# Performance work log

Hardware: AMD Instinct MI355X
Metric: run time of the kernel (lower is better)

The kernel has to match this reference:

```python
import jax, jax.numpy as jnp
import numpy as np

THRESHOLD = 20.0
CIRCLE_OFFSETS = [(0, -3), (1, -3), (2, -2), (3, -1), (3, 0), (3, 1), (2, 2), (1, 3),
                  (0, 3), (-1, 3), (-2, 2), (-3, 1), (-3, 0), (-3, -1), (-2, -2), (-1, -3)]


def setup_inputs() -> dict:
    key = jax.random.key(0)
    image = jax.random.uniform(key, (4, 1, 1080, 1920), dtype=jnp.float32) * 255.0
    return {"image": image}


def _detect_9_consecutive(bits_16):
    # bits_16: int32 (N, H, W). Build 24-bit circular buffer, test all 16 rotations
    # for 9 consecutive set bits (window == 511) using arithmetic-only ops.
    lower_8 = bits_16 % 256
    buffer_24 = bits_16 + lower_8 * 65536  # (N, H, W) int32
    divisors = (jnp.int32(2) ** jnp.arange(16, dtype=jnp.int32)).reshape(16, 1, 1, 1)
    shifted = (buffer_24[None] // divisors) % 512  # (16, N, H, W)
    return jnp.any(shifted == 511, axis=0)  # (N, H, W) bool


def reference(image):
    N, C, H, W = image.shape
    img = image.astype(jnp.float32)
    # Replicate-pad by 3 and gather the 16 Bresenham circle pixels via shifted slices.
    padded = jnp.pad(img[:, 0], ((0, 0), (3, 3), (3, 3)), mode='edge')  # (N, H+6, W+6)
    circle = jnp.stack(
        [padded[:, 3 + dy:3 + dy + H, 3 + dx:3 + dx + W] for dy, dx in CIRCLE_OFFSETS],
        axis=-1)  # (N, H, W, 16)
    center = img[:, 0][..., None]  # (N, H, W, 1)
    diff = circle - center
    powers = (jnp.int32(1) << jnp.arange(16, dtype=jnp.int32)).reshape(1, 1, 1, 16)
    dark_bits = ((diff >= THRESHOLD).astype(jnp.int32) * powers).sum(axis=-1)
    bright_bits = ((diff <= -THRESHOLD).astype(jnp.int32) * powers).sum(axis=-1)
    detected = _detect_9_consecutive(dark_bits) | _detect_9_consecutive(bright_bits)
    return detected.astype(jnp.float32)[:, None]  # (N, 1, H, W)
```

## Files before the change

### kernel.cpp

```cpp
#include <hip/hip_runtime.h>

#define IMG_H 1080
#define IMG_W 1920
#define TILE_W 128
#define TILE_H 32
#define SW 134
#define SH 38
#define SP 136

__device__ __forceinline__ unsigned det9(unsigned m) {
    unsigned x = m | (m << 16);
    unsigned t = x & (x >> 1);
    t &= t >> 2;
    t &= t >> 4;
    t &= x >> 8;
    return t & 0xFFFFu;
}

__global__ __launch_bounds__(256) void fast_score_kernel(const float* __restrict__ img,
                                                         float* __restrict__ out) {
    __shared__ float sm[SH * SP];

    const int n  = blockIdx.z;
    const int x0 = blockIdx.x * TILE_W;
    const int y0 = blockIdx.y * TILE_H;
    const int tid = threadIdx.x;

    const float* in = img + (size_t)n * (IMG_H * IMG_W);
    float* op = out + (size_t)n * (IMG_H * IMG_W);

    {
        const int lane = tid & 63;
        const int rgrp = tid >> 6;
        for (int r = rgrp; r < SH; r += 4) {
            int gy = y0 - 3 + r;
            gy = min(max(gy, 0), IMG_H - 1);
            const float* rowp = in + (size_t)gy * IMG_W;
            for (int c = lane; c < SW; c += 64) {
                int gx = x0 - 3 + c;
                gx = min(max(gx, 0), IMG_W - 1);
                sm[r * SP + c] = rowp[gx];
            }
        }
    }
    __syncthreads();

    const int cg = tid & 31;
    const int rg = tid >> 5;
    const int C = cg * 4;
    const int R = rg * 4;

    float wv[10][12];
#pragma unroll
    for (int r = 0; r < 10; ++r) {
        const float* sp = &sm[(R + r) * SP + C];
        float4 a = *(const float4*)(sp);
        float4 b = *(const float4*)(sp + 4);
        float4 c4 = *(const float4*)(sp + 8);
        wv[r][0] = a.x;  wv[r][1] = a.y;  wv[r][2]  = a.z;  wv[r][3]  = a.w;
        wv[r][4] = b.x;  wv[r][5] = b.y;  wv[r][6]  = b.z;  wv[r][7]  = b.w;
        wv[r][8] = c4.x; wv[r][9] = c4.y; wv[r][10] = c4.z; wv[r][11] = c4.w;
    }

    constexpr int DY[16] = {0, 1, 2, 3, 3, 3, 2, 1, 0, -1, -2, -3, -3, -3, -2, -1};
    constexpr int DX[16] = {-3, -3, -2, -1, 0, 1, 2, 3, 3, 3, 2, 1, 0, -1, -2, -3};

#pragma unroll
    for (int rr = 0; rr < 4; ++rr) {
        const int gy = y0 + R + rr;
        float4 res;
        float* resp = &res.x;
#pragma unroll
        for (int cc = 0; cc < 4; ++cc) {
            const float center = wv[rr + 3][cc + 3];
            unsigned dark = 0u, bright = 0u;
#pragma unroll
            for (int k = 0; k < 16; ++k) {
                const float d = wv[rr + 3 + DY[k]][cc + 3 + DX[k]] - center;
                dark   |= (d >=  20.0f ? 1u : 0u) << k;
                bright |= (d <= -20.0f ? 1u : 0u) << k;
            }
            resp[cc] = (det9(dark) | det9(bright)) ? 1.0f : 0.0f;
        }
        if (gy < IMG_H) {
            *(float4*)(op + (size_t)gy * IMG_W + (x0 + C)) = res;
        }
    }
}

extern "C" void kernel_launch(void* const* d_in, const int* in_sizes, int n_in,
                              void* d_out, int out_size, void* d_ws, size_t ws_size,
                              hipStream_t stream) {
    const float* img = (const float*)d_in[0];
    float* out = (float*)d_out;
    const int n_img = in_sizes[0] / (IMG_H * IMG_W);
    dim3 grid((IMG_W + TILE_W - 1) / TILE_W,
              (IMG_H + TILE_H - 1) / TILE_H,
              n_img);
    fast_score_kernel<<<grid, 256, 0, stream>>>(img, out);
}
```

Baseline: 114.6 us.

## Use rolling 7-row register window and precomputed thresholds in FAST kernel

Replaces the 10x12 register window with a 7-row ring buffer of float4s that is refilled from shared memory as each output row finishes, reducing live registers, and requests 4 blocks per CU through launch bounds. The threshold comparisons now test neighbours against precomputed center±20 instead of subtracting per neighbour. Bits are built by shift-in, which reverses bit order; the circular 9-run test is symmetric so the result is unchanged, and the 0xFFFF mask is dropped since only non-zero is tested. Comparing against center±20 instead of the difference may flip results on rare float rounding edge cases.

```diff
diff --git a/kernel.cpp b/kernel.cpp
--- a/kernel.cpp
+++ b/kernel.cpp
@@ -14,11 +14,20 @@
     t &= t >> 2;
     t &= t >> 4;
     t &= x >> 8;
-    return t & 0xFFFFu;
+    return t;
 }
 
-__global__ __launch_bounds__(256) void fast_score_kernel(const float* __restrict__ img,
-                                                         float* __restrict__ out) {
+__device__ __forceinline__ float elem(const float4& v, int k) {
+    switch (k & 3) {
+        case 0: return v.x;
+        case 1: return v.y;
+        case 2: return v.z;
+        default: return v.w;
+    }
+}
+
+__global__ __launch_bounds__(256, 4) void fast_score_kernel(const float* __restrict__ img,
+                                                            float* __restrict__ out) {
     __shared__ float sm[SH * SP];
 
     const int n  = blockIdx.z;
@@ -50,40 +59,49 @@
     const int C = cg * 4;
     const int R = rg * 4;
 
-    float wv[10][12];
-#pragma unroll
-    for (int r = 0; r < 10; ++r) {
-        const float* sp = &sm[(R + r) * SP + C];
-        float4 a = *(const float4*)(sp);
-        float4 b = *(const float4*)(sp + 4);
-        float4 c4 = *(const float4*)(sp + 8);
-        wv[r][0] = a.x;  wv[r][1] = a.y;  wv[r][2]  = a.z;  wv[r][3]  = a.w;
-        wv[r][4] = b.x;  wv[r][5] = b.y;  wv[r][6]  = b.z;  wv[r][7]  = b.w;
-        wv[r][8] = c4.x; wv[r][9] = c4.y; wv[r][10] = c4.z; wv[r][11] = c4.w;
-    }
-
     constexpr int DY[16] = {0, 1, 2, 3, 3, 3, 2, 1, 0, -1, -2, -3, -3, -3, -2, -1};
     constexpr int DX[16] = {-3, -3, -2, -1, 0, 1, 2, 3, 3, 3, 2, 1, 0, -1, -2, -3};
 
+    float4 w[7][3];
+
+#pragma unroll
+    for (int j = 0; j < 7; ++j) {
+        const float* sp = &sm[(R + j) * SP + C];
+        w[j][0] = *(const float4*)(sp);
+        w[j][1] = *(const float4*)(sp + 4);
+        w[j][2] = *(const float4*)(sp + 8);
+    }
+
 #pragma unroll
     for (int rr = 0; rr < 4; ++rr) {
-        const int gy = y0 + R + rr;
-        float4 res;
-        float* resp = &res.x;
+        float r[4];
 #pragma unroll
         for (int cc = 0; cc < 4; ++cc) {
-            const float center = wv[rr + 3][cc + 3];
+            const int ccol = cc + 3;
+            const float center = elem(w[(rr + 3) % 7][ccol >> 2], ccol & 3);
+            const float hi = center + 20.0f;
+            const float lo = center - 20.0f;
             unsigned dark = 0u, bright = 0u;
 #pragma unroll
             for (int k = 0; k < 16; ++k) {
-                const float d = wv[rr + 3 + DY[k]][cc + 3 + DX[k]] - center;
-                dark   |= (d >=  20.0f ? 1u : 0u) << k;
-                bright |= (d <= -20.0f ? 1u : 0u) << k;
+                const int wi = (rr + 3 + DY[k]) % 7;
+                const int col = cc + 3 + DX[k];
+                const float t = elem(w[wi][col >> 2], col & 3);
+                dark   = (dark << 1)   | (t >= hi ? 1u : 0u);
+                bright = (bright << 1) | (t <= lo ? 1u : 0u);
             }
-            resp[cc] = (det9(dark) | det9(bright)) ? 1.0f : 0.0f;
+            r[cc] = (det9(dark) | det9(bright)) ? 1.0f : 0.0f;
         }
+        const int gy = y0 + R + rr;
         if (gy < IMG_H) {
-            *(float4*)(op + (size_t)gy * IMG_W + (x0 + C)) = res;
+            *(float4*)(op + (size_t)gy * IMG_W + (x0 + C)) =
+                make_float4(r[0], r[1], r[2], r[3]);
+        }
+        if (rr < 3) {
+            const float* sp = &sm[(R + rr + 7) * SP + C];
+            w[rr % 7][0] = *(const float4*)(sp);
+            w[rr % 7][1] = *(const float4*)(sp + 4);
+            w[rr % 7][2] = *(const float4*)(sp + 8);
         }
     }
 }
```

Result: no change. 114.6 us (+0.0%).
